# Optimization experiments

Measured on AMD Instinct MI355X. Metric: run time of the kernel, lower is better.

Reference implementation:

```python
import jax, jax.numpy as jnp
import numpy as np

B, N, DIM = 4, 1024, 768
H, HD = 12, DIM // 12
GP = 49
MLP = 3072


def _layernorm(x, w, b, eps=1e-5):
    mu = x.mean(axis=-1, keepdims=True)
    var = ((x - mu) ** 2).mean(axis=-1, keepdims=True)
    return (x - mu) * jax.lax.rsqrt(var + eps) * w + b


def setup_inputs() -> dict:
    key = jax.random.key(0)
    ks = jax.random.split(key, 12)
    s = 0.02
    return {
        "x": jax.random.normal(ks[0], (B, N, DIM), jnp.float32),
        "ln1_w": jnp.ones((DIM,), jnp.float32),
        "ln1_b": jnp.zeros((DIM,), jnp.float32),
        "qkv_w": jax.random.normal(ks[1], (DIM, 3 * DIM), jnp.float32) * s,
        "qkv_b": jnp.zeros((3 * DIM,), jnp.float32),
        "proj_w": jax.random.normal(ks[2], (DIM, DIM), jnp.float32) * s,
        "proj_b": jnp.zeros((DIM,), jnp.float32),
        "gp_w": jax.random.normal(ks[3], (GP, DIM), jnp.float32) * s,  # nn.Linear(dim, gp_num).weight, shape (gp_num, dim)
        "alpha": jax.random.normal(ks[4], (1, H, 1, 1), jnp.float32),
        "ln2_w": jnp.ones((DIM,), jnp.float32),
        "ln2_b": jnp.zeros((DIM,), jnp.float32),
        "ff1_w": jax.random.normal(ks[5], (DIM, MLP), jnp.float32) * s,
        "ff1_b": jnp.zeros((MLP,), jnp.float32),
        "ff2_w": jax.random.normal(ks[6], (MLP, DIM), jnp.float32) * s,
        "ff2_b": jnp.zeros((DIM,), jnp.float32),
    }


def reference(x, ln1_w, ln1_b, qkv_w, qkv_b, proj_w, proj_b, gp_w, alpha,
              ln2_w, ln2_b, ff1_w, ff1_b, ff2_w, ff2_b):
    b, n, _ = x.shape
    # --- attention branch ---
    xn = _layernorm(x, ln1_w, ln1_b)
    qkv = xn @ qkv_w + qkv_b                                 # [b,n,3*dim]
    q, k, v = jnp.split(qkv, 3, axis=-1)
    to_heads = lambda t: t.reshape(b, n, H, HD).transpose(0, 2, 1, 3)  # [b,h,n,hd]
    q, k, v = to_heads(q), to_heads(k), to_heads(v)
    scale = HD ** -0.5
    attn = jnp.einsum('bhnd,bhmd->bhnm', q, k) * scale       # raw scores
    # group weights: view (gp_num, dim) -> (h, gp_num, hd) (row-major, same as torch .view)
    gp = gp_w.reshape(H, GP, HD)
    gw = jnp.einsum('bhnd,hmd->bhnm', v, gp)                 # [b,h,n,gp]
    gw = jax.nn.gelu(gw, approximate=False)
    gw = jax.nn.softmax(gw, axis=-1)
    gw = jnp.einsum('bhnm,bhkm->bhnk', gw, gw)               # [b,h,n,n]
    attn = jax.nn.softmax(attn * gw, axis=-1)
    a = jax.nn.sigmoid(alpha)
    attn = (1.0 - a) * attn + a * gw
    attn = attn / (attn.sum(axis=2, keepdims=True) + 1e-8)   # note: dim=2 (column renorm), faithful to source
    out = jnp.einsum('bhnm,bhmd->bhnd', attn, v)
    out = out.transpose(0, 2, 1, 3).reshape(b, n, DIM)
    out = out @ proj_w + proj_b
    x = out + x
    # --- FFN branch ---
    xn = _layernorm(x, ln2_w, ln2_b)
    hdn = jax.nn.gelu(xn @ ff1_w + ff1_b, approximate=False)
    x = (hdn @ ff2_w + ff2_b) + x
    return x
```

## Files before the change

### kernel.cpp

```cpp
#include <hip/hip_runtime.h>
#include <hip/hip_bf16.h>
#include <math.h>

#define DEVI __device__ __forceinline__

typedef __bf16 bf16x8 __attribute__((ext_vector_type(8)));
typedef float f32x4 __attribute__((ext_vector_type(4)));
typedef unsigned int u32x4 __attribute__((ext_vector_type(4)));
typedef float f32x4v __attribute__((ext_vector_type(4)));
typedef unsigned short u16;

#define WAIT_VM0 __builtin_amdgcn_s_waitcnt(0x0F70)

DEVI u16 f2bf(float f) {
    __hip_bfloat16 h = __float2bfloat16(f);
    return __builtin_bit_cast(u16, h);
}
DEVI float bf2f(u16 u) {
    unsigned int x = ((unsigned int)u) << 16;
    return __builtin_bit_cast(float, x);
}
DEVI float gelu_f(float x) { return 0.5f * x * (1.f + erff(x * 0.70710678118654752f)); }
DEVI float sigm(float x) { return 1.f / (1.f + __expf(-x)); }

DEVI bf16x8 ldfrag(const u16* p) {
    return __builtin_bit_cast(bf16x8, *reinterpret_cast<const u32x4*>(p));
}

DEVI void gload_lds16(const u16* g, u16* l) {
    __builtin_amdgcn_global_load_lds(
        (const __attribute__((address_space(1))) void*)g,
        (__attribute__((address_space(3))) void*)l, 16, 0, 0);
}

DEVI void stage8(const u16* gbase, long long stride, u16* lds, int lane) {
    int r = lane >> 3;
    int kg = (lane & 7) ^ r;
    gload_lds16(gbase + (long long)r * stride + kg * 8, lds);
}
DEVI bf16x8 fragsw(const u16* tile, int rr, int k) {
    return ldfrag(&tile[rr * 64 + ((k ^ (rr & 7)) << 3)]);
}

__global__ __launch_bounds__(256) void zero_k(float* __restrict__ p) {
    p[(long long)blockIdx.x * 256 + threadIdx.x] = 0.f;
}

__global__ __launch_bounds__(256) void tcast_k(const float* __restrict__ in, u16* __restrict__ out,
                                               int R, int C) {
    __shared__ float tile[32][33];
    int c0 = blockIdx.x * 32, r0 = blockIdx.y * 32;
    for (int ry = threadIdx.y; ry < 32; ry += 8)
        tile[ry][threadIdx.x] = in[(long long)(r0 + ry) * C + c0 + threadIdx.x];
    __syncthreads();
    for (int cy = threadIdx.y; cy < 32; cy += 8)
        out[(long long)(c0 + cy) * R + r0 + threadIdx.x] = f2bf(tile[threadIdx.x][cy]);
}

__global__ __launch_bounds__(256) void ln_k(const float* __restrict__ parts, int nparts, long long pstride,
                                            const float* __restrict__ bias2, const float* __restrict__ in2,
                                            const float* __restrict__ w, const float* __restrict__ b,
                                            u16* __restrict__ outbf, float* __restrict__ x1out) {
    int row = blockIdx.x;
    long long ro = (long long)row * 768;
    __shared__ float lds1[4], lds2[4];
    float v[3];
    float s = 0.f, sq = 0.f;
#pragma unroll
    for (int j = 0; j < 3; j++) {
        int c = threadIdx.x + j * 256;
        float x = 0.f;
        for (int p = 0; p < nparts; p++) x += parts[p * pstride + ro + c];
        if (bias2) x += bias2[c];
        if (in2) x += in2[ro + c];
        v[j] = x; s += x; sq += x * x;
    }
    if (x1out) {
#pragma unroll
        for (int j = 0; j < 3; j++) x1out[ro + threadIdx.x + j * 256] = v[j];
    }
    for (int off = 32; off; off >>= 1) { s += __shfl_down(s, off); sq += __shfl_down(sq, off); }
    int wid = threadIdx.x >> 6;
    if ((threadIdx.x & 63) == 0) { lds1[wid] = s; lds2[wid] = sq; }
    __syncthreads();
    s = lds1[0] + lds1[1] + lds1[2] + lds1[3];
    sq = lds2[0] + lds2[1] + lds2[2] + lds2[3];
    float mu = s * (1.f / 768.f);
    float var = sq * (1.f / 768.f) - mu * mu;
    float rs = rsqrtf(var + 1e-5f);
#pragma unroll
    for (int j = 0; j < 3; j++) {
        int c = threadIdx.x + j * 256;
        outbf[ro + c] = f2bf((v[j] - mu) * rs * w[c] + b[c]);
    }
}

struct GemmP {
    const u16* A; const u16* B;
    float* outF; u16* outB;
    const float* bias;
    u16* qh; u16* kh; u16* vh;
    int K, lda, ldb, ldc;
    long long pstride;
    int epi;
    int splits;
};

__global__ __launch_bounds__(256) void gemm_bt4(GemmP p) {
    __shared__ u16 As[128 * 64];
    __shared__ u16 Bs[128 * 64];
    const int tid = threadIdx.x, lane = tid & 63, wave = tid >> 6;
    const int l16 = lane & 15, qd = lane >> 4;
    const int bn0 = blockIdx.x * 128, bm0 = blockIdx.y * 128;
    const int wm0 = (wave >> 1) * 64, wn0 = (wave & 1) * 64;
    const int kc = p.K / p.splits;
    const int kbeg = blockIdx.z * kc, kend = kbeg + kc;
    f32x4 acc[4][4] = {};
    for (int k0 = kbeg; k0 < kend; k0 += 64) {
        __syncthreads();
#pragma unroll
        for (int t = 0; t < 4; t++) {
            int rowg = wave * 32 + t * 8;
            stage8(p.A + (long long)(bm0 + rowg) * p.lda + k0, p.lda, As + rowg * 64, lane);
            stage8(p.B + (long long)(bn0 + rowg) * p.ldb + k0, p.ldb, Bs + rowg * 64, lane);
        }
        __syncthreads();
#pragma unroll
        for (int s = 0; s < 2; s++) {
            bf16x8 af[4], bv[4];
#pragma unroll
            for (int i = 0; i < 4; i++) af[i] = fragsw(As, wm0 + i * 16 + l16, s * 4 + qd);
#pragma unroll
            for (int j = 0; j < 4; j++) bv[j] = fragsw(Bs, wn0 + j * 16 + l16, s * 4 + qd);
#pragma unroll
            for (int i = 0; i < 4; i++)
#pragma unroll
                for (int j = 0; j < 4; j++)
                    acc[i][j] = __builtin_amdgcn_mfma_f32_16x16x32_bf16(af[i], bv[j], acc[i][j], 0, 0, 0);
        }
    }
#pragma unroll
    for (int i = 0; i < 4; i++)
#pragma unroll
        for (int j = 0; j < 4; j++)
#pragma unroll
            for (int r = 0; r < 4; r++) {
                int row = bm0 + wm0 + i * 16 + qd * 4 + r;
                int col = bn0 + wn0 + j * 16 + l16;
                float v = acc[i][j][r];
                if (p.epi == 0) {
                    p.outF[(long long)blockIdx.z * p.pstride + (long long)row * p.ldc + col] = v;
                } else if (p.epi == 2) {
                    p.outB[(long long)row * p.ldc + col] = f2bf(gelu_f(v + p.bias[col]));
                } else {
                    v += p.bias[col];
                    int sect = col / 768, cc = col % 768;
                    int h = cc >> 6, d = cc & 63;
                    int b = row >> 10, n = row & 1023;
                    long long o = ((long long)(b * 12 + h) * 1024 + n) * 64 + d;
                    if (sect == 0) p.qh[o] = f2bf(v * 0.125f);
                    else if (sect == 1) p.kh[o] = f2bf(v);
                    else p.vh[o] = f2bf(v);
                }
            }
}

__global__ __launch_bounds__(256) void gpcast_k(const float* __restrict__ gp_w, u16* __restrict__ gpB) {
    int h = blockIdx.x;
    for (int i = threadIdx.x; i < 4096; i += 256) {
        int m = i >> 6, d = i & 63;
        float v = (m < 49) ? gp_w[h * 3136 + m * 64 + d] : 0.f;
        gpB[h * 4096 + i] = f2bf(v);
    }
}

__global__ __launch_bounds__(256) void gw0m_k(const u16* __restrict__ vh, const u16* __restrict__ gpB,
                                              u16* __restrict__ gwn) {
    __shared__ u16 As[64 * 64];
    __shared__ u16 Bs[64 * 64];
    const int tid = threadIdx.x, lane = tid & 63, wave = tid >> 6;
    const int l16 = lane & 15, qd = lane >> 4;
    const int z = blockIdx.y, n0 = blockIdx.x * 64, h = z % 12;
    const u16* vz = vh + ((long long)z * 1024 + n0) * 64;
    const u16* gz = gpB + h * 4096;
#pragma unroll
    for (int t = 0; t < 2; t++) {
        int rowg = wave * 16 + t * 8;
        stage8(vz + (long long)rowg * 64, 64, As + rowg * 64, lane);
        stage8(gz + (long long)rowg * 64, 64, Bs + rowg * 64, lane);
    }
    __syncthreads();
    f32x4 acc[4] = {};
#pragma unroll
    for (int s = 0; s < 2; s++) {
        bf16x8 af = fragsw(As, wave * 16 + l16, s * 4 + qd);
#pragma unroll
        for (int j = 0; j < 4; j++) {
            bf16x8 bv = fragsw(Bs, j * 16 + l16, s * 4 + qd);
            acc[j] = __builtin_amdgcn_mfma_f32_16x16x32_bf16(af, bv, acc[j], 0, 0, 0);
        }
    }
    float ex[4][4];
#pragma unroll
    for (int r = 0; r < 4; r++) {
        float mx = -1e30f;
        float gv[4];
#pragma unroll
        for (int j = 0; j < 4; j++) {
            int col = j * 16 + l16;
            float g = gelu_f(acc[j][r]);
            gv[j] = g;
            if (col < 49) mx = fmaxf(mx, g);
            else gv[j] = -1e30f;
        }
        mx = fmaxf(mx, __shfl_xor(mx, 1)); mx = fmaxf(mx, __shfl_xor(mx, 2));
        mx = fmaxf(mx, __shfl_xor(mx, 4)); mx = fmaxf(mx, __shfl_xor(mx, 8));
        float s = 0.f;
#pragma unroll
        for (int j = 0; j < 4; j++) {
            int col = j * 16 + l16;
            float e = (col < 49) ? __expf(gv[j] - mx) : 0.f;
            ex[r][j] = e;
            s += e;
        }
        s += __shfl_xor(s, 1); s += __shfl_xor(s, 2);
        s += __shfl_xor(s, 4); s += __shfl_xor(s, 8);
        float inv = 1.f / s;
        int row = wave * 16 + qd * 4 + r;
        long long o = ((long long)z * 1024 + n0 + row) * 64;
#pragma unroll
        for (int j = 0; j < 4; j++)
            gwn[o + j * 16 + l16] = f2bf(ex[r][j] * inv);
    }
}

__global__ __launch_bounds__(256) void attn_tg4(const u16* __restrict__ qh, const u16* __restrict__ kh,
                                                const u16* __restrict__ gwn, u16* __restrict__ e,
                                                float* __restrict__ rowsumE) {
    __shared__ u16 As[128 * 64];
    __shared__ u16 Bs[128 * 64];
    const int tid = threadIdx.x, lane = tid & 63, wave = tid >> 6;
    const int l16 = lane & 15, qd = lane >> 4;
    const int bn0 = blockIdx.x * 128, bm0 = blockIdx.y * 128, z = blockIdx.z;
    const int wm0 = (wave >> 1) * 64, wn0 = (wave & 1) * 64;
    const u16* qz = qh + (long long)z * 65536;
    const u16* kz = kh + (long long)z * 65536;
    const u16* gz = gwn + (long long)z * 65536;
    f32x4 accS[4][4] = {};
    f32x4 accG[4][4] = {};
#pragma unroll
    for (int t = 0; t < 4; t++) {
        int rowg = wave * 32 + t * 8;
        stage8(qz + (long long)(bm0 + rowg) * 64, 64, As + rowg * 64, lane);
        stage8(kz + (long long)(bn0 + rowg) * 64, 64, Bs + rowg * 64, lane);
    }
    __syncthreads();
#pragma unroll
    for (int s = 0; s < 2; s++) {
        bf16x8 af[4], bv[4];
#pragma unroll
        for (int i = 0; i < 4; i++) af[i] = fragsw(As, wm0 + i * 16 + l16, s * 4 + qd);
#pragma unroll
        for (int j = 0; j < 4; j++) bv[j] = fragsw(Bs, wn0 + j * 16 + l16, s * 4 + qd);
#pragma unroll
        for (int i = 0; i < 4; i++)
#pragma unroll
            for (int j = 0; j < 4; j++)
                accS[i][j] = __builtin_amdgcn_mfma_f32_16x16x32_bf16(af[i], bv[j], accS[i][j], 0, 0, 0);
    }
    __syncthreads();
#pragma unroll
    for (int t = 0; t < 4; t++) {
        int rowg = wave * 32 + t * 8;
        stage8(gz + (long long)(bm0 + rowg) * 64, 64, As + rowg * 64, lane);
        stage8(gz + (long long)(bn0 + rowg) * 64, 64, Bs + rowg * 64, lane);
    }
    __syncthreads();
#pragma unroll
    for (int s = 0; s < 2; s++) {
        bf16x8 af[4], bv[4];
#pragma unroll
        for (int i = 0; i < 4; i++) af[i] = fragsw(As, wm0 + i * 16 + l16, s * 4 + qd);
#pragma unroll
        for (int j = 0; j < 4; j++) bv[j] = fragsw(Bs, wn0 + j * 16 + l16, s * 4 + qd);
#pragma unroll
        for (int i = 0; i < 4; i++)
#pragma unroll
            for (int j = 0; j < 4; j++)
                accG[i][j] = __builtin_amdgcn_mfma_f32_16x16x32_bf16(af[i], bv[j], accG[i][j], 0, 0, 0);
    }
    long long zoff = (long long)z * 1048576;
#pragma unroll
    for (int i = 0; i < 4; i++)
#pragma unroll
        for (int r = 0; r < 4; r++) {
            int row = bm0 + wm0 + i * 16 + qd * 4 + r;
            float rs = 0.f;
#pragma unroll
            for (int j = 0; j < 4; j++) {
                int col = bn0 + wn0 + j * 16 + l16;
                float ev = __expf(accS[i][j][r] * accG[i][j][r]);
                e[zoff + (long long)row * 1024 + col] = f2bf(ev);
                rs += ev;
            }
            rs += __shfl_xor(rs, 1); rs += __shfl_xor(rs, 2);
            rs += __shfl_xor(rs, 4); rs += __shfl_xor(rs, 8);
            if (l16 == 0) atomicAdd(&rowsumE[z * 1024 + row], rs);
        }
}

__global__ __launch_bounds__(256) void combine2_k(const u16* __restrict__ gwn, const float* __restrict__ alpha,
                                                  float* __restrict__ colsum) {
    int z = blockIdx.x, h = z % 12;
    int j = threadIdx.x & 63, part = threadIdx.x >> 6;
    __shared__ float lds[4][64];
    __shared__ float Sl[64];
    float s = 0.f;
    for (int i = 0; i < 256; i++)
        s += bf2f(gwn[((long long)z * 1024 + part * 256 + i) * 64 + j]);
    lds[part][j] = s;
    __syncthreads();
    if (threadIdx.x < 64)
        Sl[threadIdx.x] = lds[0][threadIdx.x] + lds[1][threadIdx.x] + lds[2][threadIdx.x] + lds[3][threadIdx.x];
    __syncthreads();
    float a = sigm(alpha[h]);
    for (int m = threadIdx.x; m < 1024; m += 256) {
        const u16* g = gwn + ((long long)z * 1024 + m) * 64;
        float dot = 0.f;
#pragma unroll 8
        for (int jj = 0; jj < 64; jj++) dot += bf2f(g[jj]) * Sl[jj];
        colsum[z * 1024 + m] = a * dot;
    }
}

__global__ __launch_bounds__(256) void colsumE_k(const u16* __restrict__ e, const float* __restrict__ rowsumE,
                                                 const float* __restrict__ alpha, float* __restrict__ colsum) {
    int m = blockIdx.x * 256 + threadIdx.x;
    int n0 = blockIdx.y * 128;
    int z = blockIdx.z, h = z % 12;
    float a = sigm(alpha[h]);
    const u16* p = e + (long long)z * 1048576;
    const float* rs = rowsumE + z * 1024;
    float s = 0.f;
    for (int n = n0; n < n0 + 128; n++) s += bf2f(p[(long long)n * 1024 + m]) * (1.f / rs[n]);
    atomicAdd(&colsum[z * 1024 + m], (1.f - a) * s);
}

__global__ __launch_bounds__(256) void vpt_k(const u16* __restrict__ vh, const float* __restrict__ colsum,
                                             u16* __restrict__ vpt) {
    int z = blockIdx.y, m0 = blockIdx.x * 64;
    __shared__ float ts[64 * 65];
    int mi = threadIdx.x >> 6, d = threadIdx.x & 63;
    for (int rr = 0; rr < 16; rr++) {
        int row = rr * 4 + mi;
        ts[row * 65 + d] = bf2f(vh[((long long)z * 1024 + m0 + row) * 64 + d]);
    }
    __syncthreads();
    int mj = threadIdx.x & 63, d0 = threadIdx.x >> 6;
    for (int rr = 0; rr < 16; rr++) {
        int dd = rr * 4 + d0;
        float cs = colsum[z * 1024 + m0 + mj] + 1e-8f;
        vpt[((long long)z * 64 + dd) * 1024 + m0 + mj] = f2bf(ts[mj * 65 + dd] / cs);
    }
}

__global__ __launch_bounds__(256) void wgemm_k(const u16* __restrict__ gwn, const u16* __restrict__ vpt,
                                               float* __restrict__ Wt) {
    int z = blockIdx.y, n0 = blockIdx.x * 128;
    __shared__ u16 gs[128 * 64];
    __shared__ u16 vs2[64 * 128];
    for (int i = threadIdx.x; i < 128 * 64; i += 256) {
        int nn = i >> 6, j = i & 63;
        gs[i] = gwn[((long long)z * 1024 + n0 + nn) * 64 + j];
        int d = i >> 7, n2 = i & 127;
        vs2[i] = vpt[((long long)z * 64 + d) * 1024 + n0 + n2];
    }
    __syncthreads();
    int j = threadIdx.x & 63, dg = threadIdx.x >> 6;
    float acc[16] = {};
    for (int nn = 0; nn < 128; nn++) {
        float g = bf2f(gs[nn * 64 + j]);
#pragma unroll
        for (int i = 0; i < 16; i++) acc[i] += g * bf2f(vs2[(dg * 16 + i) * 128 + nn]);
    }
#pragma unroll
    for (int i = 0; i < 16; i++)
        atomicAdd(&Wt[((long long)z * 64 + dg * 16 + i) * 64 + j], acc[i]);
}

__global__ __launch_bounds__(256) void wtcast_k(const float* __restrict__ Wt, u16* __restrict__ WtB) {
    long long i = (long long)blockIdx.x * 256 + threadIdx.x;
    WtB[i] = f2bf(Wt[i]);
}

__global__ __launch_bounds__(64) void attn_out_1w(const u16* __restrict__ e, const u16* __restrict__ vpt,
                                                  const u16* __restrict__ gwn, const u16* __restrict__ WtB,
                                                  const float* __restrict__ rowsumE,
                                                  const float* __restrict__ alpha, u16* __restrict__ out) {
    __shared__ u16 As[64 * 64];
    __shared__ u16 Bs[64 * 64];
    const int lane = threadIdx.x;
    const int l16 = lane & 15, qd = lane >> 4;
    const int bm0 = blockIdx.x * 64, z = blockIdx.y;
    const int h = z % 12, b = z / 12;
    const u16* Pz = e + (long long)z * 1048576;
    const u16* vz = vpt + (long long)z * 65536;
    f32x4 accP[4][4] = {};
    f32x4 accG[4][4] = {};
    for (int k0 = 0; k0 < 1024; k0 += 64) {
        WAIT_VM0;
#pragma unroll
        for (int t = 0; t < 8; t++)
            stage8(Pz + (long long)(bm0 + t * 8) * 1024 + k0, 1024, As + t * 512, lane);
#pragma unroll
        for (int t = 0; t < 8; t++)
            stage8(vz + (long long)(t * 8) * 1024 + k0, 1024, Bs + t * 512, lane);
        WAIT_VM0;
#pragma unroll
        for (int s = 0; s < 2; s++) {
            bf16x8 af[4], bv[4];
#pragma unroll
            for (int ii = 0; ii < 4; ii++) af[ii] = fragsw(As, ii * 16 + l16, s * 4 + qd);
#pragma unroll
            for (int j = 0; j < 4; j++) bv[j] = fragsw(Bs, j * 16 + l16, s * 4 + qd);
#pragma unroll
            for (int ii = 0; ii < 4; ii++)
#pragma unroll
                for (int j = 0; j < 4; j++)
                    accP[ii][j] = __builtin_amdgcn_mfma_f32_16x16x32_bf16(af[ii], bv[j], accP[ii][j], 0, 0, 0);
        }
    }
    const u16* gz = gwn + (long long)z * 65536;
    const u16* wz = WtB + (long long)z * 4096;
    WAIT_VM0;
#pragma unroll
    for (int t = 0; t < 8; t++) stage8(gz + (long long)(bm0 + t * 8) * 64, 64, As + t * 512, lane);
#pragma unroll
    for (int t = 0; t < 8; t++) stage8(wz + (long long)(t * 8) * 64, 64, Bs + t * 512, lane);
    WAIT_VM0;
#pragma unroll
    for (int s = 0; s < 2; s++) {
        bf16x8 af[4], bv[4];
#pragma unroll
        for (int ii = 0; ii < 4; ii++) af[ii] = fragsw(As, ii * 16 + l16, s * 4 + qd);
#pragma unroll
        for (int j = 0; j < 4; j++) bv[j] = fragsw(Bs, j * 16 + l16, s * 4 + qd);
#pragma unroll
        for (int ii = 0; ii < 4; ii++)
#pragma unroll
            for (int j = 0; j < 4; j++)
                accG[ii][j] = __builtin_amdgcn_mfma_f32_16x16x32_bf16(af[ii], bv[j], accG[ii][j], 0, 0, 0);
    }
    float a = sigm(alpha[h]);
#pragma unroll
    for (int i = 0; i < 4; i++)
#pragma unroll
        for (int r = 0; r < 4; r++) {
            int n = bm0 + i * 16 + qd * 4 + r;
            float sc = (1.f - a) / rowsumE[z * 1024 + n];
#pragma unroll
            for (int j = 0; j < 4; j++) {
                int d = j * 16 + l16;
                float v = sc * accP[i][j][r] + a * accG[i][j][r];
                out[((long long)(b * 1024 + n)) * 768 + h * 64 + d] = f2bf(v);
            }
        }
}

__global__ __launch_bounds__(256) void fuse2_k(const float* __restrict__ parts, long long pstride4,
                                               const float* __restrict__ bias, const float* __restrict__ x1,
                                               float* __restrict__ outp) {
    long long i4 = (long long)blockIdx.x * 256 + threadIdx.x;
    int c4 = (int)(i4 % 192);
    const f32x4v* p0 = (const f32x4v*)parts;
    f32x4v v = p0[i4] + p0[pstride4 + i4] + p0[2 * pstride4 + i4] + p0[3 * pstride4 + i4];
    f32x4v bb = ((const f32x4v*)bias)[c4];
    f32x4v xx = ((const f32x4v*)x1)[i4];
    ((f32x4v*)outp)[i4] = v + bb + xx;
}

extern "C" void kernel_launch(void* const* d_in, const int* in_sizes, int n_in,
                              void* d_out, int out_size, void* d_ws, size_t ws_size,
                              hipStream_t stream) {
    const float* x      = (const float*)d_in[0];
    const float* ln1_w  = (const float*)d_in[1];
    const float* ln1_b  = (const float*)d_in[2];
    const float* qkv_w  = (const float*)d_in[3];
    const float* qkv_b  = (const float*)d_in[4];
    const float* proj_w = (const float*)d_in[5];
    const float* proj_b = (const float*)d_in[6];
    const float* gp_w   = (const float*)d_in[7];
    const float* alpha  = (const float*)d_in[8];
    const float* ln2_w  = (const float*)d_in[9];
    const float* ln2_b  = (const float*)d_in[10];
    const float* ff1_w  = (const float*)d_in[11];
    const float* ff1_b  = (const float*)d_in[12];
    const float* ff2_w  = (const float*)d_in[13];
    const float* ff2_b  = (const float*)d_in[14];

    char* w = (char*)d_ws;
    size_t off = 0;
    auto alloc = [&](size_t bytes) { size_t r = off; off += (bytes + 255) & ~(size_t)255; return r; };

    u16*   xn_bf   = (u16*)(w + alloc(4096LL * 768 * 2));
    u16*   wqkv_t  = (u16*)(w + alloc(2304LL * 768 * 2));
    u16*   wproj_t = (u16*)(w + alloc(768LL * 768 * 2));
    u16*   wff1_t  = (u16*)(w + alloc(3072LL * 768 * 2));
    u16*   wff2_t  = (u16*)(w + alloc(768LL * 3072 * 2));
    u16*   gpB     = (u16*)(w + alloc(12LL * 64 * 64 * 2));
    u16*   qh      = (u16*)(w + alloc(48LL * 1024 * 64 * 2));
    u16*   kh      = (u16*)(w + alloc(48LL * 1024 * 64 * 2));
    u16*   vh      = (u16*)(w + alloc(48LL * 1024 * 64 * 2));
    u16*   gwn     = (u16*)(w + alloc(48LL * 1024 * 64 * 2));
    u16*   ebuf    = (u16*)(w + alloc(48LL * 1024 * 1024 * 2));
    float* rowsumE = (float*)(w + alloc(48LL * 1024 * 4));
    float* Wt      = (float*)(w + alloc(48LL * 64 * 64 * 4));
    u16*   WtB     = (u16*)(w + alloc(48LL * 64 * 64 * 2));
    float* colsum  = (float*)(w + alloc(48LL * 1024 * 4));
    u16*   vpt     = (u16*)(w + alloc(48LL * 64 * 1024 * 2));
    float* x1      = (float*)(w + alloc(4096LL * 768 * 4));
    u16*   attn_o  = (u16*)(w + alloc(4096LL * 768 * 2));
    u16*   xn2     = (u16*)(w + alloc(4096LL * 768 * 2));
    float* projP = (float*)ebuf;
    u16*   hmid  = (u16*)((char*)ebuf + 2 * 4096LL * 768 * 4);
    float* ff2P  = (float*)((char*)ebuf + 2 * 4096LL * 768 * 4 + 4096LL * 3072 * 2);

    dim3 blk(256);
    dim3 wv(64);
    const long long PS = 4096LL * 768;

    tcast_k<<<dim3(72, 24), dim3(32, 8), 0, stream>>>(qkv_w, wqkv_t, 768, 2304);
    tcast_k<<<dim3(24, 24), dim3(32, 8), 0, stream>>>(proj_w, wproj_t, 768, 768);
    tcast_k<<<dim3(96, 24), dim3(32, 8), 0, stream>>>(ff1_w, wff1_t, 768, 3072);
    tcast_k<<<dim3(24, 96), dim3(32, 8), 0, stream>>>(ff2_w, wff2_t, 3072, 768);
    gpcast_k<<<dim3(12), blk, 0, stream>>>(gp_w, gpB);

    ln_k<<<dim3(4096), blk, 0, stream>>>(x, 1, 0, nullptr, nullptr, ln1_w, ln1_b, xn_bf, nullptr);

    {
        GemmP p = {xn_bf, wqkv_t, nullptr, nullptr, qkv_b, qh, kh, vh, 768, 768, 768, 0, 0, 4, 1};
        gemm_bt4<<<dim3(18, 32, 1), blk, 0, stream>>>(p);
    }

    gw0m_k<<<dim3(16, 48), blk, 0, stream>>>(vh, gpB, gwn);

    zero_k<<<dim3(192), blk, 0, stream>>>(rowsumE);
    attn_tg4<<<dim3(8, 8, 48), blk, 0, stream>>>(qh, kh, gwn, ebuf, rowsumE);

    combine2_k<<<dim3(48), blk, 0, stream>>>(gwn, alpha, colsum);
    colsumE_k<<<dim3(4, 8, 48), blk, 0, stream>>>(ebuf, rowsumE, alpha, colsum);

    vpt_k<<<dim3(16, 48), blk, 0, stream>>>(vh, colsum, vpt);

    zero_k<<<dim3(768), blk, 0, stream>>>(Wt);
    wgemm_k<<<dim3(8, 48), blk, 0, stream>>>(gwn, vpt, Wt);
    wtcast_k<<<dim3(768), blk, 0, stream>>>(Wt, WtB);

    attn_out_1w<<<dim3(16, 48), wv, 0, stream>>>(ebuf, vpt, gwn, WtB, rowsumE, alpha, attn_o);

    {
        GemmP p = {attn_o, wproj_t, projP, nullptr, nullptr, nullptr, nullptr, nullptr,
                   768, 768, 768, 768, PS, 0, 2};
        gemm_bt4<<<dim3(6, 32, 2), blk, 0, stream>>>(p);
    }

    ln_k<<<dim3(4096), blk, 0, stream>>>(projP, 2, PS, proj_b, x, ln2_w, ln2_b, xn2, x1);

    {
        GemmP p = {xn2, wff1_t, nullptr, hmid, ff1_b, nullptr, nullptr, nullptr,
                   768, 768, 768, 3072, 0, 2, 1};
        gemm_bt4<<<dim3(24, 32, 1), blk, 0, stream>>>(p);
    }

    {
        GemmP p = {hmid, wff2_t, ff2P, nullptr, nullptr, nullptr, nullptr, nullptr,
                   3072, 3072, 3072, 768, PS, 0, 4};
        gemm_bt4<<<dim3(6, 32, 4), blk, 0, stream>>>(p);
    }

    fuse2_k<<<dim3(3072), blk, 0, stream>>>(ff2P, PS / 4, ff2_b, x1, (float*)d_out);
}
```

Baseline: 502.3 us.

## Split attention output across four waves, tanh GELU, halve FF2 split-K

The attention-output kernel goes from one wave per 64-row tile to four waves per block. Each wave now owns 16 rows and shares the staged LDS tiles under block barriers, which should improve latency hiding and occupancy. The exact erf GELU is replaced by a tanh approximation, which changes numerics against the reference's exact GELU. The FF2 GEMM split-K drops from 4 to 2, so fewer partial buffers are written and summed, at the cost of less parallelism per GEMM.

```diff
diff --git a/kernel.cpp b/kernel.cpp
--- a/kernel.cpp
+++ b/kernel.cpp
@@ -10,8 +10,6 @@
 typedef float f32x4v __attribute__((ext_vector_type(4)));
 typedef unsigned short u16;
 
-#define WAIT_VM0 __builtin_amdgcn_s_waitcnt(0x0F70)
-
 DEVI u16 f2bf(float f) {
     __hip_bfloat16 h = __float2bfloat16(f);
     return __builtin_bit_cast(u16, h);
@@ -20,7 +18,12 @@
     unsigned int x = ((unsigned int)u) << 16;
     return __builtin_bit_cast(float, x);
 }
-DEVI float gelu_f(float x) { return 0.5f * x * (1.f + erff(x * 0.70710678118654752f)); }
+DEVI float gelu_f(float x) {
+    float y = 0.7978845608f * (x + 0.044715f * x * x * x);
+    float e = __expf(2.f * y);
+    float t = 1.f - 2.f / (e + 1.f);
+    return 0.5f * x * (1.f + t);
+}
 DEVI float sigm(float x) { return 1.f / (1.f + __expf(-x)); }
 
 DEVI bf16x8 ldfrag(const u16* p) {
@@ -393,78 +396,71 @@
     WtB[i] = f2bf(Wt[i]);
 }
 
-__global__ __launch_bounds__(64) void attn_out_1w(const u16* __restrict__ e, const u16* __restrict__ vpt,
-                                                  const u16* __restrict__ gwn, const u16* __restrict__ WtB,
-                                                  const float* __restrict__ rowsumE,
-                                                  const float* __restrict__ alpha, u16* __restrict__ out) {
+__global__ __launch_bounds__(256) void attn_out4(const u16* __restrict__ e, const u16* __restrict__ vpt,
+                                                 const u16* __restrict__ gwn, const u16* __restrict__ WtB,
+                                                 const float* __restrict__ rowsumE,
+                                                 const float* __restrict__ alpha, u16* __restrict__ out) {
     __shared__ u16 As[64 * 64];
     __shared__ u16 Bs[64 * 64];
-    const int lane = threadIdx.x;
+    const int tid = threadIdx.x, lane = tid & 63, wave = tid >> 6;
     const int l16 = lane & 15, qd = lane >> 4;
     const int bm0 = blockIdx.x * 64, z = blockIdx.y;
     const int h = z % 12, b = z / 12;
     const u16* Pz = e + (long long)z * 1048576;
     const u16* vz = vpt + (long long)z * 65536;
-    f32x4 accP[4][4] = {};
-    f32x4 accG[4][4] = {};
+    const int wr = wave * 16;
+    f32x4 accP[4] = {};
+    f32x4 accG[4] = {};
     for (int k0 = 0; k0 < 1024; k0 += 64) {
-        WAIT_VM0;
-#pragma unroll
-        for (int t = 0; t < 8; t++)
-            stage8(Pz + (long long)(bm0 + t * 8) * 1024 + k0, 1024, As + t * 512, lane);
-#pragma unroll
-        for (int t = 0; t < 8; t++)
-            stage8(vz + (long long)(t * 8) * 1024 + k0, 1024, Bs + t * 512, lane);
-        WAIT_VM0;
+        __syncthreads();
+#pragma unroll
+        for (int t = 0; t < 2; t++) {
+            int rowg = wave * 16 + t * 8;
+            stage8(Pz + (long long)(bm0 + rowg) * 1024 + k0, 1024, As + rowg * 64, lane);
+            stage8(vz + (long long)rowg * 1024 + k0, 1024, Bs + rowg * 64, lane);
+        }
+        __syncthreads();
 #pragma unroll
         for (int s = 0; s < 2; s++) {
-            bf16x8 af[4], bv[4];
-#pragma unroll
-            for (int ii = 0; ii < 4; ii++) af[ii] = fragsw(As, ii * 16 + l16, s * 4 + qd);
-#pragma unroll
-            for (int j = 0; j < 4; j++) bv[j] = fragsw(Bs, j * 16 + l16, s * 4 + qd);
-#pragma unroll
-            for (int ii = 0; ii < 4; ii++)
-#pragma unroll
-                for (int j = 0; j < 4; j++)
-                    accP[ii][j] = __builtin_amdgcn_mfma_f32_16x16x32_bf16(af[ii], bv[j], accP[ii][j], 0, 0, 0);
+            bf16x8 af = fragsw(As, wr + l16, s * 4 + qd);
+#pragma unroll
+            for (int j = 0; j < 4; j++) {
+                bf16x8 bv = fragsw(Bs, j * 16 + l16, s * 4 + qd);
+                accP[j] = __builtin_amdgcn_mfma_f32_16x16x32_bf16(af, bv, accP[j], 0, 0, 0);
+            }
         }
     }
     const u16* gz = gwn + (long long)z * 65536;
     const u16* wz = WtB + (long long)z * 4096;
-    WAIT_VM0;
-#pragma unroll
-    for (int t = 0; t < 8; t++) stage8(gz + (long long)(bm0 + t * 8) * 64, 64, As + t * 512, lane);
-#pragma unroll
-    for (int t = 0; t < 8; t++) stage8(wz + (long long)(t * 8) * 64, 64, Bs + t * 512, lane);
-    WAIT_VM0;
+    __syncthreads();
+#pragma unroll
+    for (int t = 0; t < 2; t++) {
+        int rowg = wave * 16 + t * 8;
+        stage8(gz + (long long)(bm0 + rowg) * 64, 64, As + rowg * 64, lane);
+        stage8(wz + (long long)rowg * 64, 64, Bs + rowg * 64, lane);
+    }
+    __syncthreads();
 #pragma unroll
     for (int s = 0; s < 2; s++) {
-        bf16x8 af[4], bv[4];
-#pragma unroll
-        for (int ii = 0; ii < 4; ii++) af[ii] = fragsw(As, ii * 16 + l16, s * 4 + qd);
-#pragma unroll
-        for (int j = 0; j < 4; j++) bv[j] = fragsw(Bs, j * 16 + l16, s * 4 + qd);
-#pragma unroll
-        for (int ii = 0; ii < 4; ii++)
-#pragma unroll
-            for (int j = 0; j < 4; j++)
-                accG[ii][j] = __builtin_amdgcn_mfma_f32_16x16x32_bf16(af[ii], bv[j], accG[ii][j], 0, 0, 0);
+        bf16x8 af = fragsw(As, wr + l16, s * 4 + qd);
+#pragma unroll
+        for (int j = 0; j < 4; j++) {
+            bf16x8 bv = fragsw(Bs, j * 16 + l16, s * 4 + qd);
+            accG[j] = __builtin_amdgcn_mfma_f32_16x16x32_bf16(af, bv, accG[j], 0, 0, 0);
+        }
     }
     float a = sigm(alpha[h]);
 #pragma unroll
-    for (int i = 0; i < 4; i++)
-#pragma unroll
-        for (int r = 0; r < 4; r++) {
-            int n = bm0 + i * 16 + qd * 4 + r;
-            float sc = (1.f - a) / rowsumE[z * 1024 + n];
-#pragma unroll
-            for (int j = 0; j < 4; j++) {
-                int d = j * 16 + l16;
-                float v = sc * accP[i][j][r] + a * accG[i][j][r];
-                out[((long long)(b * 1024 + n)) * 768 + h * 64 + d] = f2bf(v);
-            }
-        }
+    for (int r = 0; r < 4; r++) {
+        int n = bm0 + wr + qd * 4 + r;
+        float sc = (1.f - a) / rowsumE[z * 1024 + n];
+#pragma unroll
+        for (int j = 0; j < 4; j++) {
+            int d = j * 16 + l16;
+            float v = sc * accP[j][r] + a * accG[j][r];
+            out[((long long)(b * 1024 + n)) * 768 + h * 64 + d] = f2bf(v);
+        }
+    }
 }
 
 __global__ __launch_bounds__(256) void fuse2_k(const float* __restrict__ parts, long long pstride4,
@@ -473,7 +469,7 @@
     long long i4 = (long long)blockIdx.x * 256 + threadIdx.x;
     int c4 = (int)(i4 % 192);
     const f32x4v* p0 = (const f32x4v*)parts;
-    f32x4v v = p0[i4] + p0[pstride4 + i4] + p0[2 * pstride4 + i4] + p0[3 * pstride4 + i4];
+    f32x4v v = p0[i4] + p0[pstride4 + i4];
     f32x4v bb = ((const f32x4v*)bias)[c4];
     f32x4v xx = ((const f32x4v*)x1)[i4];
     ((f32x4v*)outp)[i4] = v + bb + xx;
@@ -526,7 +522,6 @@
     float* ff2P  = (float*)((char*)ebuf + 2 * 4096LL * 768 * 4 + 4096LL * 3072 * 2);
 
     dim3 blk(256);
-    dim3 wv(64);
     const long long PS = 4096LL * 768;
 
     tcast_k<<<dim3(72, 24), dim3(32, 8), 0, stream>>>(qkv_w, wqkv_t, 768, 2304);
@@ -556,7 +551,7 @@
     wgemm_k<<<dim3(8, 48), blk, 0, stream>>>(gwn, vpt, Wt);
     wtcast_k<<<dim3(768), blk, 0, stream>>>(Wt, WtB);
 
-    attn_out_1w<<<dim3(16, 48), wv, 0, stream>>>(ebuf, vpt, gwn, WtB, rowsumE, alpha, attn_o);
+    attn_out4<<<dim3(16, 48), blk, 0, stream>>>(ebuf, vpt, gwn, WtB, rowsumE, alpha, attn_o);
 
     {
         GemmP p = {attn_o, wproj_t, projP, nullptr, nullptr, nullptr, nullptr, nullptr,
@@ -574,8 +569,8 @@
 
     {
         GemmP p = {hmid, wff2_t, ff2P, nullptr, nullptr, nullptr, nullptr, nullptr,
-                   3072, 3072, 3072, 768, PS, 0, 4};
-        gemm_bt4<<<dim3(6, 32, 4), blk, 0, stream>>>(p);
+                   3072, 3072, 3072, 768, PS, 0, 2};
+        gemm_bt4<<<dim3(6, 32, 2), blk, 0, stream>>>(p);
     }
 
     fuse2_k<<<dim3(3072), blk, 0, stream>>>(ff2P, PS / 4, ff2_b, x1, (float*)d_out);
```

Result: faster. 480.9 us (-4.3%).
